# Performance work log

Measured on AMD Instinct MI355X. Metric: run time of the kernel, lower is better.

The kernel has to match this reference:

```python
import jax, jax.numpy as jnp
import numpy as np

H, K, D, HID, B = 8, 2048, 64, 1024, 8192
TEMP = 1.0
LN_EPS = 1e-5


def setup_inputs() -> dict:
    key = jax.random.key(0)
    ks = jax.random.split(key, 6)
    s = lambda k, shape, scale=0.02: jax.random.normal(k, shape, jnp.float32) * scale
    return dict(
        z=jax.random.normal(ks[0], (B, HID), jnp.float32),
        w1=s(ks[1], (H, HID, 2 * D)),
        b1=jnp.zeros((H, 2 * D), jnp.float32),
        w2=s(ks[2], (H, 2 * D, D)),
        b2=jnp.zeros((H, D), jnp.float32),
        ln_g=jnp.ones((H, D), jnp.float32),
        ln_b=jnp.zeros((H, D), jnp.float32),
        codebooks=jax.random.normal(ks[3], (H, K, D), jnp.float32) * 0.1,
        dec_w=s(ks[4], (H, D, HID // H)),
        dec_b=jnp.zeros((H, HID // H), jnp.float32),
    )


def reference(z, w1, b1, w2, b2, ln_g, ln_b, codebooks, dec_w, dec_b):
    sg = jax.lax.stop_gradient
    Bf = z.shape[0]
    # per-head projection MLP (all heads fused via einsum): [B,HID] -> [B,H,2D] -> [B,H,D]
    h1 = jax.nn.gelu(jnp.einsum('bi,hio->bho', z, w1) + b1, approximate=False)
    zh = jnp.einsum('bho,hod->bhd', h1, w2) + b2
    mu = zh.mean(-1, keepdims=True)
    var = zh.var(-1, keepdims=True)  # biased, as torch LayerNorm
    z_heads = (zh - mu) / jnp.sqrt(var + LN_EPS) * ln_g + ln_b  # [B,H,D]
    # squared-distance to codebooks: ||z||^2 + ||c||^2 - 2 z.c  -> [B,H,K]
    z_sq = (z_heads ** 2).sum(-1)[..., None]          # [B,H,1]
    c_sq = (codebooks ** 2).sum(-1)[None]             # [1,H,K]
    zc = jnp.einsum('bhd,hkd->bhk', z_heads, codebooks)
    dists = z_sq + c_sq - 2.0 * zc
    idx = jnp.argmin(dists, axis=-1)                  # [B,H] int
    z_q = codebooks[jnp.arange(H)[None, :], idx]      # gather -> [B,H,D]
    # per-head decoders then concat -> [B,HID]
    dec = lambda x: (jnp.einsum('bhd,hdo->bho', x, dec_w) + dec_b).reshape(Bf, -1)
    z_q_dec = dec(z_q)
    z_proj = dec(z_heads)
    z_q_st = z_proj + sg(z_q_dec - z_proj)
    commit = jnp.mean((z_proj - sg(z_q_dec)) ** 2)
    codebook_loss = jnp.mean((sg(z_proj) - z_q_dec) ** 2)
    # entropy regularizer over soft assignment probs
    probs = jax.nn.softmax(-dists * TEMP, axis=-1)    # [B,H,K]
    avg_probs = probs.mean(0)                         # [H,K]
    entropy = -(avg_probs * jnp.log(avg_probs + 1e-8)).sum(-1).mean()
    entropy_loss = 1.0 - entropy / np.float32(np.log(K))
    # orthogonality: pairwise co-occurrence deviation from independence
    p = jnp.zeros((H, K), jnp.float32).at[jnp.arange(H)[None, :], idx].add(1.0) / Bf  # [H,K]
    ortho = jnp.float32(0.0)
    cnt = 0
    for i in range(H):
        for j in range(i + 1, H):
            co = jnp.zeros((K, K), jnp.float32).at[idx[:, i], idx[:, j]].add(1.0) / (Bf + 1e-8)
            expected = p[i][:, None] * p[j][None, :]
            ortho = ortho + jnp.mean(jnp.abs(co - expected))
            cnt += 1
    ortho = ortho / cnt
    return z_q_st, idx, commit, codebook_loss, entropy_loss, ortho, sg(z_heads)
```

## Files before the change

kernel.cpp:

```cpp
#include <hip/hip_runtime.h>
#include <math.h>

#define H 8
#define KK 2048
#define DD 64
#define HIDN 1024
#define BB 8192
#define TWO_D 128
#define OO 128

#define WS_CSQ   1048576
#define WS_ZSQ   1064960
#define WS_IDX   1130496
#define WS_AVGP  1196032
#define WS_HIST  1212416
#define WS_ACC   1228800
#define WS_ZERO_BYTES ((16384 + 16384 + 4) * 4)

#define OUT_ZQ 0
#define OUT_IDX 8388608
#define OUT_COMMIT 8454144
#define OUT_CBL 8454145
#define OUT_ENT 8454146
#define OUT_ORTHO 8454147
#define OUT_ZH 8454148
#define W2P_OFF 3145728

typedef __attribute__((ext_vector_type(8))) short bf16x8;
typedef __attribute__((ext_vector_type(4))) float f32x4;

__device__ inline unsigned short bf16_rne(float x) {
    union { float f; unsigned u; } c; c.f = x;
    unsigned r = c.u + 0x7FFFu + ((c.u >> 16) & 1u);
    return (unsigned short)(r >> 16);
}
__device__ inline float bf16_f32(unsigned short h) {
    union { unsigned u; float f; } c; c.u = ((unsigned)h) << 16;
    return c.f;
}
__device__ inline void split3(float x, short* hh, short* mm, short* ll) {
    unsigned short h_ = bf16_rne(x);
    float r1 = x - bf16_f32(h_);
    unsigned short m_ = bf16_rne(r1);
    float r2 = r1 - bf16_f32(m_);
    unsigned short l_ = bf16_rne(r2);
    *hh = (short)h_; *mm = (short)m_; *ll = (short)l_;
}

__device__ inline void gload_lds16(const void* g, void* l) {
    __builtin_amdgcn_global_load_lds(
        (const __attribute__((address_space(1))) unsigned int*)g,
        (__attribute__((address_space(3))) unsigned int*)l, 16, 0, 0);
}

__global__ __launch_bounds__(256) void k_pre_w1(const float* __restrict__ w1, float* outp) {
    short* w1p = (short*)outp;
    int h = blockIdx.x >> 5, kc = blockIdx.x & 31;
    int t = threadIdx.x;
    int l = t & 63, w = t >> 6;
    int lb = l & 15, lg = l >> 4;
#pragma unroll
    for (int oi = 0; oi < 2; ++oi) {
        int ot = w + oi * 4;
        union { short e[8]; bf16x8 v; } uh, um, ul;
#pragma unroll
        for (int j = 0; j < 8; ++j) {
            float x = w1[(size_t)(h * HIDN + kc * 32 + lg * 8 + j) * TWO_D + ot * 16 + lb];
            split3(x, &uh.e[j], &um.e[j], &ul.e[j]);
        }
        size_t base = (((size_t)(h * 32 + kc) * 8 + ot) * 3) * 512 + l * 8;
        *(bf16x8*)(w1p + base) = uh.v;
        *(bf16x8*)(w1p + base + 512) = um.v;
        *(bf16x8*)(w1p + base + 1024) = ul.v;
    }
}

__global__ __launch_bounds__(256) void k_pre_w2(const float* __restrict__ w2, float* outp) {
    short* w2p = (short*)outp + W2P_OFF;
    int h = blockIdx.x;
    int t = threadIdx.x;
    int l = t & 63, w = t >> 6;
    int lb = l & 15, lg = l >> 4;
#pragma unroll
    for (int i = 0; i < 4; ++i) {
        int fr = w * 4 + i;
        int dt = fr >> 2, oc = fr & 3;
        union { short e[8]; bf16x8 v; } uh, um, ul;
#pragma unroll
        for (int j = 0; j < 8; ++j) {
            float x = w2[(size_t)(h * TWO_D + oc * 32 + lg * 8 + j) * DD + dt * 16 + lb];
            split3(x, &uh.e[j], &um.e[j], &ul.e[j]);
        }
        size_t base = (((size_t)(h * 4 + dt) * 4 + oc) * 3) * 512 + l * 8;
        *(bf16x8*)(w2p + base) = uh.v;
        *(bf16x8*)(w2p + base + 512) = um.v;
        *(bf16x8*)(w2p + base + 1024) = ul.v;
    }
}

__global__ __launch_bounds__(256) void k_pre(const float* __restrict__ cb, float* __restrict__ ws) {
    int h = blockIdx.x >> 3, kb = blockIdx.x & 7;
    int t = threadIdx.x;
    int l = t & 63;
    int lb = l & 15, lg = l >> 4;
    short* stg = (short*)ws;
#pragma unroll
    for (int p = 0; p < 4; ++p) {
        int T = kb * 16 + p * 4 + (t >> 6);
        int k = T * 16 + lb;
        const float* row = cb + (size_t)(h * KK + k) * DD;
        float4 a0 = *(const float4*)(row + lg * 8);
        float4 a1 = *(const float4*)(row + lg * 8 + 4);
        float4 c0 = *(const float4*)(row + 32 + lg * 8);
        float4 c1 = *(const float4*)(row + 32 + lg * 8 + 4);
        float v0[8] = {a0.x, a0.y, a0.z, a0.w, a1.x, a1.y, a1.z, a1.w};
        float v1[8] = {c0.x, c0.y, c0.z, c0.w, c1.x, c1.y, c1.z, c1.w};
        union { short e[8]; bf16x8 v; } h0, h1;
        float s = 0.f;
#pragma unroll
        for (int j = 0; j < 8; ++j) {
            float x = v0[j];
            s = fmaf(x, x, s);
            h0.e[j] = (short)bf16_rne(x);
            float y = v1[j];
            s = fmaf(y, y, s);
            h1.e[j] = (short)bf16_rne(y);
        }
        int off = (T & 15) * 8 + (T >> 4);
        size_t base = ((size_t)(h * 128 + off)) * 1024 + l * 8;
        *(bf16x8*)(stg + base) = h0.v;
        *(bf16x8*)(stg + base + 512) = h1.v;
        s += __shfl_xor(s, 16);
        s += __shfl_xor(s, 32);
        if (lg == 0) ws[WS_CSQ + h * KK + k] = s;
    }
}

__global__ __launch_bounds__(512, 4) void k1(const float* __restrict__ z, const float* __restrict__ b1,
                                             const float* __restrict__ b2, const float* __restrict__ lng,
                                             const float* __restrict__ lnb, float* out,
                                             float* __restrict__ ws) {
    __shared__ char SM[51200];
    int t = threadIdx.x;
    int h = blockIdx.y;
    int b0 = blockIdx.x * 64;
    int w = t >> 6, l = t & 63;
    int rg = w >> 1, wc = w & 1;
    int lb = l & 15, lg = l >> 4;

    const short* w2p = (const short*)out + W2P_OFF;
    const char* w1h = (const char*)out + (size_t)h * (32 * 24576);
    const float* zrow = z + (size_t)(b0 + rg * 16 + lb) * HIDN + lg * 8;

    {
        char* lb0 = SM + (t >> 6) * 1024;
        const char* gb = w1h + t * 16;
#pragma unroll
        for (int r = 0; r < 3; ++r) gload_lds16(gb + r * 8192, lb0 + r * 8192);
#pragma unroll
        for (int r = 0; r < 3; ++r) gload_lds16(gb + 24576 + r * 8192, lb0 + 24576 + r * 8192);
    }
    float4 zA = *(const float4*)(zrow);
    float4 zB = *(const float4*)(zrow + 4);
    __syncthreads();

    f32x4 acc[4];
#pragma unroll
    for (int i = 0; i < 4; ++i) acc[i] = (f32x4){0.f, 0.f, 0.f, 0.f};

#pragma unroll
    for (int c = 0; c < 32; ++c) {
        if (c > 0) {
            if (c < 31) asm volatile("s_waitcnt vmcnt(3)" ::: "memory");
            else        asm volatile("s_waitcnt vmcnt(0)" ::: "memory");
            __builtin_amdgcn_sched_barrier(0);
            __builtin_amdgcn_s_barrier();
            __builtin_amdgcn_sched_barrier(0);
        }
        {
            float zc[8] = {zA.x, zA.y, zA.z, zA.w, zB.x, zB.y, zB.z, zB.w};
            union { short e[8]; bf16x8 v; } uh, um, ul;
#pragma unroll
            for (int j = 0; j < 8; ++j) split3(zc[j], &uh.e[j], &um.e[j], &ul.e[j]);
            bf16x8 bh = uh.v, bm = um.v, blo = ul.v;
            const char* bp = SM + (c & 1) * 24576;
#pragma unroll
            for (int ot = 0; ot < 4; ++ot) {
                const char* fb = bp + (wc * 4 + ot) * 3072 + l * 16;
                bf16x8 ah = *(const bf16x8*)(fb);
                bf16x8 am = *(const bf16x8*)(fb + 1024);
                bf16x8 al = *(const bf16x8*)(fb + 2048);
                f32x4 cc = acc[ot];
                cc = __builtin_amdgcn_mfma_f32_16x16x32_bf16(ah, bh, cc, 0, 0, 0);
                cc = __builtin_amdgcn_mfma_f32_16x16x32_bf16(ah, bm, cc, 0, 0, 0);
                cc = __builtin_amdgcn_mfma_f32_16x16x32_bf16(am, bh, cc, 0, 0, 0);
                cc = __builtin_amdgcn_mfma_f32_16x16x32_bf16(ah, blo, cc, 0, 0, 0);
                cc = __builtin_amdgcn_mfma_f32_16x16x32_bf16(al, bh, cc, 0, 0, 0);
                cc = __builtin_amdgcn_mfma_f32_16x16x32_bf16(am, bm, cc, 0, 0, 0);
                acc[ot] = cc;
            }
        }
        __builtin_amdgcn_sched_barrier(0);
        __builtin_amdgcn_s_barrier();
        __builtin_amdgcn_sched_barrier(0);
        if (c < 31) {
            zA = *(const float4*)(zrow + (c + 1) * 32);
            zB = *(const float4*)(zrow + (c + 1) * 32 + 4);
        }
        if (c + 2 < 32) {
            char* lb0 = SM + (c & 1) * 24576 + (t >> 6) * 1024;
            const char* gb = w1h + (size_t)(c + 2) * 24576 + t * 16;
#pragma unroll
            for (int r = 0; r < 3; ++r) gload_lds16(gb + r * 8192, lb0 + r * 8192);
        }
    }
    __syncthreads();

    float* h1L = (float*)SM;
    float* zhL = (float*)(SM + 33792);

#pragma unroll
    for (int ot = 0; ot < 4; ++ot)
#pragma unroll
        for (int r = 0; r < 4; ++r) {
            int o = (wc * 4 + ot) * 16 + lg * 4 + r;
            float x = acc[ot][r] + b1[h * TWO_D + o];
            float gl = 0.5f * x * (1.0f + erff(x * 0.70710678118654752f));
            h1L[(rg * 16 + lb) * 132 + o] = gl;
        }
    __syncthreads();

    f32x4 a2[2];
    a2[0] = (f32x4){0.f, 0.f, 0.f, 0.f};
    a2[1] = (f32x4){0.f, 0.f, 0.f, 0.f};
#pragma unroll
    for (int oc = 0; oc < 4; ++oc) {
        const float* hr = h1L + (rg * 16 + lb) * 132 + oc * 32 + lg * 8;
        union { short e[8]; bf16x8 v; } uh, um, ul;
#pragma unroll
        for (int j = 0; j < 8; ++j) split3(hr[j], &uh.e[j], &um.e[j], &ul.e[j]);
        bf16x8 bh = uh.v, bm = um.v, blo = ul.v;
#pragma unroll
        for (int dti = 0; dti < 2; ++dti) {
            int dt = wc * 2 + dti;
            const short* fb = w2p + (((size_t)(h * 4 + dt) * 4 + oc) * 3) * 512 + l * 8;
            bf16x8 ah = *(const bf16x8*)(fb);
            bf16x8 am = *(const bf16x8*)(fb + 512);
            bf16x8 al = *(const bf16x8*)(fb + 1024);
            f32x4 cc = a2[dti];
            cc = __builtin_amdgcn_mfma_f32_16x16x32_bf16(ah, bh, cc, 0, 0, 0);
            cc = __builtin_amdgcn_mfma_f32_16x16x32_bf16(ah, bm, cc, 0, 0, 0);
            cc = __builtin_amdgcn_mfma_f32_16x16x32_bf16(am, bh, cc, 0, 0, 0);
            cc = __builtin_amdgcn_mfma_f32_16x16x32_bf16(ah, blo, cc, 0, 0, 0);
            cc = __builtin_amdgcn_mfma_f32_16x16x32_bf16(al, bh, cc, 0, 0, 0);
            cc = __builtin_amdgcn_mfma_f32_16x16x32_bf16(am, bm, cc, 0, 0, 0);
            a2[dti] = cc;
        }
    }
#pragma unroll
    for (int dti = 0; dti < 2; ++dti)
#pragma unroll
        for (int r = 0; r < 4; ++r) {
            int d = (wc * 2 + dti) * 16 + lg * 4 + r;
            zhL[(rg * 16 + lb) * 68 + d] = a2[dti][r] + b2[h * DD + d];
        }
    __syncthreads();

    {
        int row = t >> 3, c0 = (t & 7) * 8;
        const float* zr = zhL + row * 68 + c0;
        float v[8];
#pragma unroll
        for (int j = 0; j < 8; ++j) v[j] = zr[j];
        float s = 0.f;
#pragma unroll
        for (int j = 0; j < 8; ++j) s += v[j];
        s += __shfl_xor(s, 1); s += __shfl_xor(s, 2); s += __shfl_xor(s, 4);
        float mu = s * (1.0f / 64.0f);
        float vv = 0.f;
#pragma unroll
        for (int j = 0; j < 8; ++j) { float d = v[j] - mu; vv = fmaf(d, d, vv); }
        vv += __shfl_xor(vv, 1); vv += __shfl_xor(vv, 2); vv += __shfl_xor(vv, 4);
        float rstd = 1.0f / sqrtf(vv * (1.0f / 64.0f) + 1e-5f);
        float zn[8]; float ss = 0.f;
#pragma unroll
        for (int j = 0; j < 8; ++j) {
            float x = (v[j] - mu) * rstd * lng[h * DD + c0 + j] + lnb[h * DD + c0 + j];
            zn[j] = x; ss = fmaf(x, x, ss);
        }
        ss += __shfl_xor(ss, 1); ss += __shfl_xor(ss, 2); ss += __shfl_xor(ss, 4);
        int brow = b0 + row;
        if ((t & 7) == 0) ws[WS_ZSQ + brow * H + h] = ss;
        float4 s0 = {zn[0], zn[1], zn[2], zn[3]};
        float4 s1 = {zn[4], zn[5], zn[6], zn[7]};
        *(float4*)(out + OUT_ZH + (size_t)(brow * H + h) * DD + c0) = s0;
        *(float4*)(out + OUT_ZH + (size_t)(brow * H + h) * DD + c0 + 4) = s1;
    }
}

#define MARGIN 0.10f
__device__ inline void stage16k(const char* gsrc, short* lbuf, int t) {
    char* lb_ = (char*)lbuf + (t >> 6) * 1024;
    const char* gb = gsrc + t * 16;
    gload_lds16(gb, lb_);
    gload_lds16(gb + 8192, lb_ + 8192);
}
__global__ __launch_bounds__(512, 4) void k2(const float* __restrict__ cb,
                                             float* __restrict__ out, float* __restrict__ ws) {
    __shared__ short bufs[3][8192];
    __shared__ float zt[16][68];
    __shared__ float redM[8][16], redS[8][16], redE[8][16];
    __shared__ int   redK[8][16];
    __shared__ float MbL[16], SbL[16];
    __shared__ float zsqL[16];

    int t = threadIdx.x;
    int h = blockIdx.y;
    int b0 = blockIdx.x * 16;
    int kg = t >> 6, l = t & 63;
    int lb = l & 15, lg = l >> 4;

    const char* stgbase = (const char*)ws + (size_t)h * 262144;

    stage16k(stgbase, bufs[0], t);
    stage16k(stgbase + 16384, bufs[1], t);
    stage16k(stgbase + 32768, bufs[2], t);
#pragma unroll
    for (int i = 0; i < 2; ++i) {
        int q = t + i * 512;
        int r = q >> 6, d = q & 63;
        zt[r][d] = out[OUT_ZH + (size_t)((b0 + r) * H + h) * DD + d];
    }
    if (t < 16) zsqL[t] = ws[WS_ZSQ + (b0 + t) * H + h];
    __syncthreads();

    bf16x8 bh[2], blo[2];
#pragma unroll
    for (int s = 0; s < 2; ++s) {
        const float* zr = &zt[lb][s * 32 + lg * 8];
        union { short e[8]; bf16x8 v; } uh, ul;
#pragma unroll
        for (int j = 0; j < 8; ++j) {
            float x = zr[j];
            unsigned short hb = bf16_rne(x);
            uh.e[j] = (short)hb;
            ul.e[j] = (short)bf16_rne(x - bf16_f32(hb));
        }
        bh[s] = uh.v; blo[s] = ul.v;
    }

    f32x4 acc[16];
#pragma unroll
    for (int a = 0; a < 16; ++a) acc[a] = (f32x4){0.f, 0.f, 0.f, 0.f};

#pragma unroll
    for (int c = 0; c < 16; ++c) {
        if (c > 0) {
            if (c <= 13)      asm volatile("s_waitcnt vmcnt(4)" ::: "memory");
            else if (c == 14) asm volatile("s_waitcnt vmcnt(2)" ::: "memory");
            else              asm volatile("s_waitcnt vmcnt(0)" ::: "memory");
            __builtin_amdgcn_sched_barrier(0);
            __builtin_amdgcn_s_barrier();
            __builtin_amdgcn_sched_barrier(0);
        }
        {
            const short* fb = bufs[c % 3] + kg * 1024 + l * 8;
            bf16x8 C0 = *(const bf16x8*)(fb);
            bf16x8 C1 = *(const bf16x8*)(fb + 512);
            f32x4 cc = acc[c];
            __builtin_amdgcn_s_setprio(1);
            cc = __builtin_amdgcn_mfma_f32_16x16x32_bf16(bh[0], C0, cc, 0, 0, 0);
            cc = __builtin_amdgcn_mfma_f32_16x16x32_bf16(blo[0], C0, cc, 0, 0, 0);
            cc = __builtin_amdgcn_mfma_f32_16x16x32_bf16(bh[1], C1, cc, 0, 0, 0);
            cc = __builtin_amdgcn_mfma_f32_16x16x32_bf16(blo[1], C1, cc, 0, 0, 0);
            __builtin_amdgcn_s_setprio(0);
            acc[c] = cc;
        }
        if (c < 15) {
            __builtin_amdgcn_sched_barrier(0);
            __builtin_amdgcn_s_barrier();
            __builtin_amdgcn_sched_barrier(0);
            if (c + 3 < 16)
                stage16k(stgbase + (size_t)(c + 3) * 16384, bufs[c % 3], t);
        }
    }

    float zsqv[4];
#pragma unroll
    for (int r = 0; r < 4; ++r) zsqv[r] = zsqL[lg * 4 + r];
    float mn[4] = {3.4e38f, 3.4e38f, 3.4e38f, 3.4e38f};
#pragma unroll
    for (int ai = 0; ai < 16; ++ai) {
        float cs = ws[WS_CSQ + h * KK + kg * 256 + ai * 16 + lb];
        f32x4 a = acc[ai];
        f32x4 d;
#pragma unroll
        for (int r = 0; r < 4; ++r) {
            float dv = (zsqv[r] + cs) - 2.f * a[r];
            d[r] = dv;
            mn[r] = fminf(mn[r], dv);
        }
        acc[ai] = d;
    }
#pragma unroll
    for (int off = 1; off < 16; off <<= 1)
#pragma unroll
        for (int r = 0; r < 4; ++r) mn[r] = fminf(mn[r], __shfl_xor(mn[r], off));
    if (lb == 0)
#pragma unroll
        for (int r = 0; r < 4; ++r) redM[kg][lg * 4 + r] = mn[r];
    __syncthreads();
    if (t < 16) {
        float m = redM[0][t];
#pragma unroll
        for (int g = 1; g < 8; ++g) m = fminf(m, redM[g][t]);
        MbL[t] = m;
    }
    __syncthreads();
    float Mb[4];
#pragma unroll
    for (int r = 0; r < 4; ++r) Mb[r] = MbL[lg * 4 + r];

    float S[4] = {0.f, 0.f, 0.f, 0.f};
    unsigned mk0 = 0, mk1 = 0, mk2 = 0, mk3 = 0;
#pragma unroll
    for (int ai = 0; ai < 16; ++ai) {
        f32x4 d = acc[ai];
        f32x4 e;
#pragma unroll
        for (int r = 0; r < 4; ++r) {
            float dv = d[r];
            float ev = __expf(Mb[r] - dv);
            S[r] += ev;
            e[r] = ev;
            bool cand = dv <= Mb[r] + MARGIN;
            if (r == 0) mk0 |= cand ? (1u << ai) : 0u;
            if (r == 1) mk1 |= cand ? (1u << ai) : 0u;
            if (r == 2) mk2 |= cand ? (1u << ai) : 0u;
            if (r == 3) mk3 |= cand ? (1u << ai) : 0u;
        }
        acc[ai] = e;
    }
#pragma unroll
    for (int off = 1; off < 16; off <<= 1)
#pragma unroll
        for (int r = 0; r < 4; ++r) S[r] += __shfl_xor(S[r], off);
    if (lb == 0)
#pragma unroll
        for (int r = 0; r < 4; ++r) redS[kg][lg * 4 + r] = S[r];

    float eB[4] = {3.4e38f, 3.4e38f, 3.4e38f, 3.4e38f};
    int kB[4] = {0x7FFFFFFF, 0x7FFFFFFF, 0x7FFFFFFF, 0x7FFFFFFF};
#pragma unroll
    for (int r = 0; r < 4; ++r) {
        unsigned m = (r == 0) ? mk0 : (r == 1) ? mk1 : (r == 2) ? mk2 : mk3;
        const float* zr0 = &zt[lg * 4 + r][0];
        float eBest = 3.4e38f; int kBest = 0x7FFFFFFF;
        while (m) {
            int ai = (int)__ffs(m) - 1;
            m &= m - 1;
            int k = kg * 256 + ai * 16 + lb;
            const float4* crow = (const float4*)(cb + (size_t)(h * KK + k) * DD);
            float s = 0.f;
#pragma unroll 1
            for (int q = 0; q < 16; ++q) {
                float4 cv = crow[q];
                s = fmaf(zr0[q * 4 + 0], cv.x, s);
                s = fmaf(zr0[q * 4 + 1], cv.y, s);
                s = fmaf(zr0[q * 4 + 2], cv.z, s);
                s = fmaf(zr0[q * 4 + 3], cv.w, s);
            }
            float ex = (zsqv[r] + ws[WS_CSQ + h * KK + k]) - 2.f * s;
            if (ex < eBest || (ex == eBest && k < kBest)) { eBest = ex; kBest = k; }
        }
        eB[r] = eBest; kB[r] = kBest;
    }
#pragma unroll
    for (int off = 1; off < 16; off <<= 1)
#pragma unroll
        for (int r = 0; r < 4; ++r) {
            float oe = __shfl_xor(eB[r], off);
            int ok = __shfl_xor(kB[r], off);
            if (oe < eB[r] || (oe == eB[r] && ok < kB[r])) { eB[r] = oe; kB[r] = ok; }
        }
    if (lb == 0)
#pragma unroll
        for (int r = 0; r < 4; ++r) {
            redE[kg][lg * 4 + r] = eB[r];
            redK[kg][lg * 4 + r] = kB[r];
        }
    __syncthreads();
    if (t < 16) {
        float Sv = redS[0][t];
#pragma unroll
        for (int g = 1; g < 8; ++g) Sv += redS[g][t];
        SbL[t] = Sv;
        float e0 = redE[0][t]; int k0_ = redK[0][t];
#pragma unroll
        for (int g = 1; g < 8; ++g) {
            float oe = redE[g][t]; int ok = redK[g][t];
            if (oe < e0 || (oe == e0 && ok < k0_)) { e0 = oe; k0_ = ok; }
        }
        out[OUT_IDX + (b0 + t) * H + h] = (float)k0_;
        ((int*)ws)[WS_IDX + (b0 + t) * H + h] = k0_;
    }
    __syncthreads();
    float invS[4];
#pragma unroll
    for (int r = 0; r < 4; ++r) invS[r] = 1.0f / SbL[lg * 4 + r];

#pragma unroll
    for (int ai = 0; ai < 16; ++ai) {
        f32x4 e = acc[ai];
        float v = e[0] * invS[0];
        v = fmaf(e[1], invS[1], v);
        v = fmaf(e[2], invS[2], v);
        v = fmaf(e[3], invS[3], v);
        v += __shfl_xor(v, 16);
        v += __shfl_xor(v, 32);
        if (lg == 0)
            atomicAdd(ws + WS_AVGP + h * KK + kg * 256 + ai * 16 + lb, v);
    }
}

__global__ __launch_bounds__(256) void k_hist(float* __restrict__ ws) {
    __shared__ unsigned hl[2048];
    int h = blockIdx.x, t = threadIdx.x;
    for (int i = t; i < 2048; i += 256) hl[i] = 0u;
    __syncthreads();
    const int* idxi = ((const int*)ws) + WS_IDX;
    for (int b = t; b < BB; b += 256)
        atomicAdd(&hl[idxi[b * H + h]], 1u);
    __syncthreads();
    for (int i = t; i < 2048; i += 256)
        ((unsigned*)ws)[WS_HIST + h * KK + i] = hl[i];
}

__global__ __launch_bounds__(256, 2) void k3(const float* __restrict__ cb, const float* __restrict__ dw,
                                             const float* __restrict__ db, float* __restrict__ out,
                                             float* __restrict__ ws) {
    __shared__ float zqt[32][65];
    __shared__ float zht[32][65];
    __shared__ float dwt[64][128];
    __shared__ int idxs[32];
    __shared__ double redc[4];
    int t = threadIdx.x;
    int h = blockIdx.y;
    int b0 = blockIdx.x * 32;
    if (t < 32) idxs[t] = ((const int*)ws)[WS_IDX + (b0 + t) * H + h];
    __syncthreads();
#pragma unroll
    for (int p = 0; p < 8; ++p) {
        int q = t + 256 * p;
        int r = q >> 6, d = q & 63;
        zqt[r][d] = cb[(size_t)(h * KK + idxs[r]) * DD + d];
        zht[r][d] = out[OUT_ZH + (size_t)((b0 + r) * H + h) * DD + d];
    }
#pragma unroll
    for (int p = 0; p < 8; ++p) {
        int q = t + 256 * p;
        int r = q >> 5, c4 = q & 31;
        *(float4*)(&dwt[r][c4 * 4]) = *(const float4*)(dw + (size_t)(h * DD + r) * OO + c4 * 4);
    }
    __syncthreads();
    int rg = t >> 4, cg = t & 15;
    float aq[2][8], ap[2][8];
#pragma unroll
    for (int i = 0; i < 2; ++i)
#pragma unroll
        for (int j = 0; j < 8; ++j) { aq[i][j] = 0.f; ap[i][j] = 0.f; }
#pragma unroll 4
    for (int d = 0; d < 64; ++d) {
        float q0 = zqt[rg * 2][d], q1 = zqt[rg * 2 + 1][d];
        float p0 = zht[rg * 2][d], p1 = zht[rg * 2 + 1][d];
        float4 wa = *(const float4*)(&dwt[d][cg * 8]);
        float4 wb = *(const float4*)(&dwt[d][cg * 8 + 4]);
        float ww[8] = {wa.x, wa.y, wa.z, wa.w, wb.x, wb.y, wb.z, wb.w};
#pragma unroll
        for (int j = 0; j < 8; ++j) {
            aq[0][j] = fmaf(q0, ww[j], aq[0][j]);
            aq[1][j] = fmaf(q1, ww[j], aq[1][j]);
            ap[0][j] = fmaf(p0, ww[j], ap[0][j]);
            ap[1][j] = fmaf(p1, ww[j], ap[1][j]);
        }
    }
    float lsum = 0.f;
#pragma unroll
    for (int i = 0; i < 2; ++i) {
        float vq4[8];
#pragma unroll
        for (int j = 0; j < 8; ++j) {
            float bb = db[h * OO + cg * 8 + j];
            float vq = aq[i][j] + bb;
            float vp = ap[i][j] + bb;
            vq4[j] = vp + (vq - vp);
            float e = vp - vq;
            lsum = fmaf(e, e, lsum);
        }
        float4 s0 = {vq4[0], vq4[1], vq4[2], vq4[3]};
        float4 s1 = {vq4[4], vq4[5], vq4[6], vq4[7]};
        size_t o = (size_t)(b0 + rg * 2 + i) * HIDN + h * OO + cg * 8;
        *(float4*)(out + OUT_ZQ + o) = s0;
        *(float4*)(out + OUT_ZQ + o + 4) = s1;
    }
#pragma unroll
    for (int off = 1; off < 64; off <<= 1) lsum += __shfl_xor(lsum, off);
    if ((t & 63) == 0) redc[t >> 6] = (double)lsum;
    __syncthreads();
    if (t == 0) atomicAdd((double*)(ws + WS_ACC), redc[0] + redc[1] + redc[2] + redc[3]);
}

__global__ __launch_bounds__(256) void k6(float* __restrict__ ws) {
    __shared__ unsigned slots[16384];
    __shared__ unsigned cnts[16384];
    int t = threadIdx.x;
    int bid = blockIdx.x;
    int pi = 0, pj = 1;
    {
        int c = 0;
        for (int a = 0; a < H; ++a)
            for (int b = a + 1; b < H; ++b) { if (c == bid) { pi = a; pj = b; } ++c; }
    }
    for (int s = t; s < 16384; s += 256) { slots[s] = 0xFFFFFFFFu; cnts[s] = 0u; }
    __syncthreads();
    const int* idxi = ((const int*)ws) + WS_IDX;
    for (int b = t; b < BB; b += 256) {
        unsigned key = ((unsigned)idxi[b * H + pi] << 11) | (unsigned)idxi[b * H + pj];
        unsigned p = (key * 2654435761u) >> 18;
        while (true) {
            unsigned old = atomicCAS(&slots[p], 0xFFFFFFFFu, key);
            if (old == 0xFFFFFFFFu || old == key) { atomicAdd(&cnts[p], 1u); break; }
            p = (p + 1) & 16383u;
        }
    }
    __syncthreads();
    const unsigned* hist = ((const unsigned*)ws) + WS_HIST;
    double loc = 0.0;
    for (int s = t; s < 16384; s += 256) {
        unsigned key = slots[s];
        if (key != 0xFFFFFFFFu) {
            int ki = (int)(key >> 11), kj = (int)(key & 2047u);
            float c = (float)cnts[s] * (1.0f / 8192.0f);
            float piv = (float)hist[pi * KK + ki] * (1.0f / 8192.0f);
            float pjv = (float)hist[pj * KK + kj] * (1.0f / 8192.0f);
            float e = piv * pjv;
            loc += (double)fabsf(c - e) - (double)e;
        }
    }
    double spi = 0.0, spj = 0.0;
    for (int k = t; k < KK; k += 256) {
        spi += (double)hist[pi * KK + k];
        spj += (double)hist[pj * KK + k];
    }
#pragma unroll
    for (int off = 1; off < 64; off <<= 1) {
        loc += __shfl_xor(loc, off);
        spi += __shfl_xor(spi, off);
        spj += __shfl_xor(spj, off);
    }
    __syncthreads();
    double* sc = (double*)cnts;
    if ((t & 63) == 0) { int w = t >> 6; sc[w] = loc; sc[4 + w] = spi; sc[8 + w] = spj; }
    __syncthreads();
    if (t == 0) {
        double L = sc[0] + sc[1] + sc[2] + sc[3];
        double SPI = (sc[4] + sc[5] + sc[6] + sc[7]) / 8192.0;
        double SPJ = (sc[8] + sc[9] + sc[10] + sc[11]) / 8192.0;
        atomicAdd(((double*)(ws + WS_ACC)) + 1, L + SPI * SPJ);
    }
}

__global__ __launch_bounds__(256) void k4(float* __restrict__ out, float* __restrict__ ws) {
    __shared__ double red[256];
    int t = threadIdx.x;
    double tot = 0.0;
    for (int h = 0; h < H; ++h) {
        double s = 0.0;
        for (int k = t; k < KK; k += 256) {
            double a = (double)ws[WS_AVGP + h * KK + k] / 8192.0;
            s += a * log(a + 1e-8);
        }
        tot += s;
    }
    red[t] = tot;
    __syncthreads();
    for (int off = 128; off; off >>= 1) {
        if (t < off) red[t] += red[t + off];
        __syncthreads();
    }
    if (t == 0) {
        double entropy = -red[0] / 8.0;
        out[OUT_ENT] = (float)(1.0 - entropy / log(2048.0));
        double ca = *(const double*)(ws + WS_ACC);
        float cm = (float)(ca / (8192.0 * 1024.0));
        out[OUT_COMMIT] = cm;
        out[OUT_CBL] = cm;
        double oa = *(((const double*)(ws + WS_ACC)) + 1);
        out[OUT_ORTHO] = (float)(oa / (28.0 * 4194304.0));
    }
}

extern "C" void kernel_launch(void* const* d_in, const int* in_sizes, int n_in,
                              void* d_out, int out_size, void* d_ws, size_t ws_size,
                              hipStream_t stream) {
    (void)in_sizes; (void)n_in; (void)out_size; (void)ws_size;
    const float* z   = (const float*)d_in[0];
    const float* w1  = (const float*)d_in[1];
    const float* b1  = (const float*)d_in[2];
    const float* w2  = (const float*)d_in[3];
    const float* b2  = (const float*)d_in[4];
    const float* lng = (const float*)d_in[5];
    const float* lnb = (const float*)d_in[6];
    const float* cb  = (const float*)d_in[7];
    const float* dw  = (const float*)d_in[8];
    const float* db  = (const float*)d_in[9];
    float* out = (float*)d_out;
    float* ws = (float*)d_ws;

    hipMemsetAsync(ws + WS_AVGP, 0, WS_ZERO_BYTES, stream);
    k_pre_w1<<<256, 256, 0, stream>>>(w1, out);
    k_pre_w2<<<8, 256, 0, stream>>>(w2, out);
    k_pre<<<64, 256, 0, stream>>>(cb, ws);
    k1<<<dim3(128, 8), 512, 0, stream>>>(z, b1, b2, lng, lnb, out, ws);
    k2<<<dim3(512, 8), 512, 0, stream>>>(cb, out, ws);
    k_hist<<<8, 256, 0, stream>>>(ws);
    k3<<<dim3(256, 8), 256, 0, stream>>>(cb, dw, db, out, ws);
    k6<<<28, 256, 0, stream>>>(ws);
    k4<<<1, 256, 0, stream>>>(out, ws);
}
```

Baseline: 568.3 us.

## Split codebook into hi/lo bf16 for distance MFMAs and tighten rescore margin

The codebook is now pre-staged as both high and low bf16 parts, and the distance GEMM adds two extra MFMAs per chunk (z_hi·c_lo) for a near-fp32 dot product. With more accurate distances, the candidate margin for exact fp32 rescoring drops from 0.10 to 0.05, so fewer scattered codebook rows are re-read. Staging doubles to 32KB per chunk with a double buffer instead of a triple buffer. The avg-probs atomic accumulation now runs before the rescoring loop. The trade-off is more MFMA work, twice the staged bandwidth and less prefetch depth, in exchange for cutting the divergent rescoring tail.

Result: slower. 588.2 us (+3.5%).

```diff
diff --git a/kernel.cpp b/kernel.cpp
--- a/kernel.cpp
+++ b/kernel.cpp
@@ -115,21 +115,26 @@
         float4 c1 = *(const float4*)(row + 32 + lg * 8 + 4);
         float v0[8] = {a0.x, a0.y, a0.z, a0.w, a1.x, a1.y, a1.z, a1.w};
         float v1[8] = {c0.x, c0.y, c0.z, c0.w, c1.x, c1.y, c1.z, c1.w};
-        union { short e[8]; bf16x8 v; } h0, h1;
+        union { short e[8]; bf16x8 v; } h0, h1, l0, l1;
         float s = 0.f;
 #pragma unroll
         for (int j = 0; j < 8; ++j) {
             float x = v0[j];
             s = fmaf(x, x, s);
-            h0.e[j] = (short)bf16_rne(x);
+            unsigned short hb = bf16_rne(x);
+            h0.e[j] = (short)hb;
+            l0.e[j] = (short)bf16_rne(x - bf16_f32(hb));
             float y = v1[j];
             s = fmaf(y, y, s);
-            h1.e[j] = (short)bf16_rne(y);
-        }
-        int off = (T & 15) * 8 + (T >> 4);
-        size_t base = ((size_t)(h * 128 + off)) * 1024 + l * 8;
+            unsigned short hb2 = bf16_rne(y);
+            h1.e[j] = (short)hb2;
+            l1.e[j] = (short)bf16_rne(y - bf16_f32(hb2));
+        }
+        size_t base = (((size_t)(h * 16 + (T & 15)) * 8) + (T >> 4)) * 2048 + l * 8;
         *(bf16x8*)(stg + base) = h0.v;
         *(bf16x8*)(stg + base + 512) = h1.v;
+        *(bf16x8*)(stg + base + 1024) = l0.v;
+        *(bf16x8*)(stg + base + 1536) = l1.v;
         s += __shfl_xor(s, 16);
         s += __shfl_xor(s, 32);
         if (lg == 0) ws[WS_CSQ + h * KK + k] = s;
@@ -298,16 +303,18 @@
     }
 }
 
-#define MARGIN 0.10f
-__device__ inline void stage16k(const char* gsrc, short* lbuf, int t) {
+#define MARGIN 0.05f
+__device__ inline void stage32k(const char* gsrc, short* lbuf, int t) {
     char* lb_ = (char*)lbuf + (t >> 6) * 1024;
     const char* gb = gsrc + t * 16;
     gload_lds16(gb, lb_);
     gload_lds16(gb + 8192, lb_ + 8192);
+    gload_lds16(gb + 16384, lb_ + 16384);
+    gload_lds16(gb + 24576, lb_ + 24576);
 }
 __global__ __launch_bounds__(512, 4) void k2(const float* __restrict__ cb,
                                              float* __restrict__ out, float* __restrict__ ws) {
-    __shared__ short bufs[3][8192];
+    __shared__ short bufs[2][16384];
     __shared__ float zt[16][68];
     __shared__ float redM[8][16], redS[8][16], redE[8][16];
     __shared__ int   redK[8][16];
@@ -320,11 +327,10 @@
     int kg = t >> 6, l = t & 63;
     int lb = l & 15, lg = l >> 4;
 
-    const char* stgbase = (const char*)ws + (size_t)h * 262144;
-
-    stage16k(stgbase, bufs[0], t);
-    stage16k(stgbase + 16384, bufs[1], t);
-    stage16k(stgbase + 32768, bufs[2], t);
+    const char* stgbase = (const char*)ws + (size_t)h * 524288;
+
+    stage32k(stgbase, bufs[0], t);
+    stage32k(stgbase + 32768, bufs[1], t);
 #pragma unroll
     for (int i = 0; i < 2; ++i) {
         int q = t + i * 512;
@@ -356,23 +362,26 @@
 #pragma unroll
     for (int c = 0; c < 16; ++c) {
         if (c > 0) {
-            if (c <= 13)      asm volatile("s_waitcnt vmcnt(4)" ::: "memory");
-            else if (c == 14) asm volatile("s_waitcnt vmcnt(2)" ::: "memory");
-            else              asm volatile("s_waitcnt vmcnt(0)" ::: "memory");
+            if (c < 15) asm volatile("s_waitcnt vmcnt(4)" ::: "memory");
+            else        asm volatile("s_waitcnt vmcnt(0)" ::: "memory");
             __builtin_amdgcn_sched_barrier(0);
             __builtin_amdgcn_s_barrier();
             __builtin_amdgcn_sched_barrier(0);
         }
         {
-            const short* fb = bufs[c % 3] + kg * 1024 + l * 8;
-            bf16x8 C0 = *(const bf16x8*)(fb);
-            bf16x8 C1 = *(const bf16x8*)(fb + 512);
+            const short* fb = bufs[c & 1] + kg * 2048 + l * 8;
+            bf16x8 C0h = *(const bf16x8*)(fb);
+            bf16x8 C1h = *(const bf16x8*)(fb + 512);
+            bf16x8 C0l = *(const bf16x8*)(fb + 1024);
+            bf16x8 C1l = *(const bf16x8*)(fb + 1536);
             f32x4 cc = acc[c];
             __builtin_amdgcn_s_setprio(1);
-            cc = __builtin_amdgcn_mfma_f32_16x16x32_bf16(bh[0], C0, cc, 0, 0, 0);
-            cc = __builtin_amdgcn_mfma_f32_16x16x32_bf16(blo[0], C0, cc, 0, 0, 0);
-            cc = __builtin_amdgcn_mfma_f32_16x16x32_bf16(bh[1], C1, cc, 0, 0, 0);
-            cc = __builtin_amdgcn_mfma_f32_16x16x32_bf16(blo[1], C1, cc, 0, 0, 0);
+            cc = __builtin_amdgcn_mfma_f32_16x16x32_bf16(bh[0], C0h, cc, 0, 0, 0);
+            cc = __builtin_amdgcn_mfma_f32_16x16x32_bf16(blo[0], C0h, cc, 0, 0, 0);
+            cc = __builtin_amdgcn_mfma_f32_16x16x32_bf16(bh[0], C0l, cc, 0, 0, 0);
+            cc = __builtin_amdgcn_mfma_f32_16x16x32_bf16(bh[1], C1h, cc, 0, 0, 0);
+            cc = __builtin_amdgcn_mfma_f32_16x16x32_bf16(blo[1], C1h, cc, 0, 0, 0);
+            cc = __builtin_amdgcn_mfma_f32_16x16x32_bf16(bh[1], C1l, cc, 0, 0, 0);
             __builtin_amdgcn_s_setprio(0);
             acc[c] = cc;
         }
@@ -380,8 +389,8 @@
             __builtin_amdgcn_sched_barrier(0);
             __builtin_amdgcn_s_barrier();
             __builtin_amdgcn_sched_barrier(0);
-            if (c + 3 < 16)
-                stage16k(stgbase + (size_t)(c + 3) * 16384, bufs[c % 3], t);
+            if (c + 2 < 16)
+                stage32k(stgbase + (size_t)(c + 2) * 32768, bufs[c & 1], t);
         }
     }
 
@@ -391,7 +400,7 @@
     float mn[4] = {3.4e38f, 3.4e38f, 3.4e38f, 3.4e38f};
 #pragma unroll
     for (int ai = 0; ai < 16; ++ai) {
-        float cs = ws[WS_CSQ + h * KK + kg * 256 + ai * 16 + lb];
+        float cs = ws[WS_CSQ + h * KK + (kg * 16 + ai) * 16 + lb];
         f32x4 a = acc[ai];
         f32x4 d;
 #pragma unroll
@@ -448,6 +457,30 @@
     if (lb == 0)
 #pragma unroll
         for (int r = 0; r < 4; ++r) redS[kg][lg * 4 + r] = S[r];
+    __syncthreads();
+    if (t < 16) {
+        float Sv = redS[0][t];
+#pragma unroll
+        for (int g = 1; g < 8; ++g) Sv += redS[g][t];
+        SbL[t] = Sv;
+    }
+    __syncthreads();
+    float invS[4];
+#pragma unroll
+    for (int r = 0; r < 4; ++r) invS[r] = 1.0f / SbL[lg * 4 + r];
+
+#pragma unroll
+    for (int ai = 0; ai < 16; ++ai) {
+        f32x4 e = acc[ai];
+        float v = e[0] * invS[0];
+        v = fmaf(e[1], invS[1], v);
+        v = fmaf(e[2], invS[2], v);
+        v = fmaf(e[3], invS[3], v);
+        v += __shfl_xor(v, 16);
+        v += __shfl_xor(v, 32);
+        if (lg == 0)
+            atomicAdd(ws + WS_AVGP + h * KK + (kg * 16 + ai) * 16 + lb, v);
+    }
 
     float eB[4] = {3.4e38f, 3.4e38f, 3.4e38f, 3.4e38f};
     int kB[4] = {0x7FFFFFFF, 0x7FFFFFFF, 0x7FFFFFFF, 0x7FFFFFFF};
@@ -459,7 +492,7 @@
         while (m) {
             int ai = (int)__ffs(m) - 1;
             m &= m - 1;
-            int k = kg * 256 + ai * 16 + lb;
+            int k = (kg * 16 + ai) * 16 + lb;
             const float4* crow = (const float4*)(cb + (size_t)(h * KK + k) * DD);
             float s = 0.f;
 #pragma unroll 1
@@ -491,10 +524,6 @@
         }
     __syncthreads();
     if (t < 16) {
-        float Sv = redS[0][t];
-#pragma unroll
-        for (int g = 1; g < 8; ++g) Sv += redS[g][t];
-        SbL[t] = Sv;
         float e0 = redE[0][t]; int k0_ = redK[0][t];
 #pragma unroll
         for (int g = 1; g < 8; ++g) {
@@ -503,23 +532,6 @@
         }
         out[OUT_IDX + (b0 + t) * H + h] = (float)k0_;
         ((int*)ws)[WS_IDX + (b0 + t) * H + h] = k0_;
-    }
-    __syncthreads();
-    float invS[4];
-#pragma unroll
-    for (int r = 0; r < 4; ++r) invS[r] = 1.0f / SbL[lg * 4 + r];
-
-#pragma unroll
-    for (int ai = 0; ai < 16; ++ai) {
-        f32x4 e = acc[ai];
-        float v = e[0] * invS[0];
-        v = fmaf(e[1], invS[1], v);
-        v = fmaf(e[2], invS[2], v);
-        v = fmaf(e[3], invS[3], v);
-        v += __shfl_xor(v, 16);
-        v += __shfl_xor(v, 32);
-        if (lg == 0)
-            atomicAdd(ws + WS_AVGP + h * KK + kg * 256 + ai * 16 + lb, v);
     }
 }
 
```
